# Kernel optimization log

Measured on AMD Instinct MI355X. Metric: run time of the kernel, lower is better.

The kernel has to match this reference:

```python
import jax, jax.numpy as jnp
import numpy as np

N, E, T, D, M, G = 131072, 524288, 4, 128, 256, 4096
VOCAB, GH, L, PASSES = 100, 512, 128, 4


def setup_inputs() -> dict:
    key = jax.random.key(0)
    ks = jax.random.split(key, 20)
    node_types = jax.random.randint(ks[0], (N,), 0, VOCAB)
    edge_src = jax.random.randint(ks[1], (E,), 0, N)
    edge_dst = jax.random.randint(ks[2], (E,), 0, N)
    edge_type = jax.random.randint(ks[3], (E,), 0, T)
    inner = jnp.sort(jax.random.randint(ks[4], (G - 1,), 0, N))
    ptr = jnp.concatenate([jnp.zeros((1,), jnp.int64 if inner.dtype == jnp.int64 else jnp.int32),
                           inner, jnp.full((1,), N, inner.dtype)])
    s = 1.0 / np.sqrt(D)
    emb = jax.random.normal(ks[5], (VOCAB, D), jnp.float32)
    W_msg = jax.random.normal(ks[6], (T, M, D), jnp.float32) * s
    b_msg = jax.random.normal(ks[7], (T, M), jnp.float32) * s
    W_ih = jax.random.normal(ks[8], (3 * D, M), jnp.float32) * (1.0 / np.sqrt(M))
    W_hh = jax.random.normal(ks[9], (3 * D, D), jnp.float32) * s
    b_ih = jax.random.normal(ks[10], (3 * D,), jnp.float32) * s
    b_hh = jax.random.normal(ks[11], (3 * D,), jnp.float32) * s
    W_gate = jax.random.normal(ks[12], (1, D), jnp.float32) * s
    b_gate = jax.random.normal(ks[13], (1,), jnp.float32) * s
    W_n2g = jax.random.normal(ks[14], (GH, D), jnp.float32) * s
    b_n2g = jax.random.normal(ks[15], (GH,), jnp.float32) * s
    W_loc = jax.random.normal(ks[16], (L, GH), jnp.float32) * (1.0 / np.sqrt(GH))
    b_loc = jax.random.normal(ks[17], (L,), jnp.float32) * (1.0 / np.sqrt(GH))
    W_lv = jax.random.normal(ks[18], (L, GH), jnp.float32) * (1.0 / np.sqrt(GH))
    b_lv = jax.random.normal(ks[19], (L,), jnp.float32) * (1.0 / np.sqrt(GH))
    return dict(node_types=node_types, edge_src=edge_src, edge_dst=edge_dst,
                edge_type=edge_type, ptr=ptr, emb=emb, W_msg=W_msg, b_msg=b_msg,
                W_ih=W_ih, W_hh=W_hh, b_ih=b_ih, b_hh=b_hh, W_gate=W_gate,
                b_gate=b_gate, W_n2g=W_n2g, b_n2g=b_n2g, W_loc=W_loc, b_loc=b_loc,
                W_lv=W_lv, b_lv=b_lv)


def _ggnn_pass(h, edge_src, edge_dst, edge_type, W_msg, b_msg, W_ih, W_hh, b_ih, b_hh):
    # per-edge-type linear on all nodes: [T, N, M]
    msgs_all = jnp.einsum('nd,tmd->tnm', h, W_msg) + b_msg[:, None, :]
    # gather the message of the edge's type at its source node: [E, M]
    e_msg = msgs_all[edge_type, edge_src]
    # sparse adjacency matmul == scatter-add of source messages into destinations
    agg = jax.ops.segment_sum(e_msg, edge_dst, num_segments=h.shape[0])
    m = jax.nn.relu(agg)
    # torch GRUCell
    gi = m @ W_ih.T + b_ih      # [N, 3D]
    gh = h @ W_hh.T + b_hh      # [N, 3D]
    d = h.shape[1]
    ir, iz, inn = gi[:, :d], gi[:, d:2 * d], gi[:, 2 * d:]
    hr, hz, hn = gh[:, :d], gh[:, d:2 * d], gh[:, 2 * d:]
    r = jax.nn.sigmoid(ir + hr)
    z = jax.nn.sigmoid(iz + hz)
    n = jnp.tanh(inn + r * hn)
    return (1.0 - z) * n + z * h


def reference(node_types, edge_src, edge_dst, edge_type, ptr, emb, W_msg, b_msg,
              W_ih, W_hh, b_ih, b_hh, W_gate, b_gate, W_n2g, b_n2g,
              W_loc, b_loc, W_lv, b_lv):
    h = emb[node_types]  # [N, D]
    for _ in range(PASSES):
        h = _ggnn_pass(h, edge_src, edge_dst, edge_type,
                       W_msg, b_msg, W_ih, W_hh, b_ih, b_hh)
    # gated segment readout (equivalent to per-graph attn @ h slices)
    gate = jax.nn.sigmoid(h @ W_gate.T + b_gate)        # [N, 1]
    hg = h @ W_n2g.T + b_n2g                            # [N, GH]
    seg = jnp.searchsorted(ptr, jnp.arange(h.shape[0]), side='right') - 1
    h_graph = jax.ops.segment_sum(gate * hg, seg, num_segments=ptr.shape[0] - 1)
    z_loc = h_graph @ W_loc.T + b_loc
    z_logvar = h_graph @ W_lv.T + b_lv
    return (z_loc, z_logvar)
```

## Files before the change

### kernel.cpp

```cpp
#include <hip/hip_runtime.h>
#include <cstdint>
#include <cstddef>

#define NN 131072
#define EE 524288
#define GG 4096
#define NPASS 4

typedef __attribute__((ext_vector_type(4))) float f32x4;
typedef __attribute__((ext_vector_type(8))) short bfrag;

__device__ __forceinline__ unsigned short f2bf(float f) {
  union { float f; unsigned u; } v; v.f = f;
  unsigned r = v.u + 0x7fffu + ((v.u >> 16) & 1u);
  return (unsigned short)(r >> 16);
}
__device__ __forceinline__ float bf2f(unsigned short h) {
  union { unsigned u; float f; } v; v.u = ((unsigned)h) << 16;
  return v.f;
}
__device__ __forceinline__ unsigned pack2(float x, float y) {
  return (unsigned)f2bf(x) | ((unsigned)f2bf(y) << 16);
}
__device__ __forceinline__ float sigm(float x) { return 1.f / (1.f + __expf(-x)); }
__device__ __forceinline__ float sigm_fast(float x) {
  return __builtin_amdgcn_rcpf(1.f + __expf(-x));
}
__device__ __forceinline__ float tanh_fast(float x) {
  return 1.f - 2.f * __builtin_amdgcn_rcpf(1.f + __expf(2.f * x));
}

__device__ __forceinline__ void cp16(unsigned short* l, const unsigned short* g) {
  __builtin_amdgcn_global_load_lds(
      (const __attribute__((address_space(1))) unsigned int*)g,
      (__attribute__((address_space(3))) unsigned int*)l, 16, 0, 0);
}

__global__ void prep_wb(const float* __restrict__ Wmsg, unsigned short* __restrict__ Wb) {
  int idx = blockIdx.x * 256 + threadIdx.x;
  if (idx >= 256 * 512) return;
  int m = idx >> 9, k = idx & 511;
  int t = k >> 7, d = k & 127;
  Wb[idx] = f2bf(Wmsg[((size_t)t * 256 + m) * 128 + d]);
}

__global__ void prep_wgru(const float* __restrict__ Wih, const float* __restrict__ Whh,
                          unsigned short* __restrict__ Wgru) {
  int idx = blockIdx.x * 256 + threadIdx.x;
  if (idx >= 512 * 384) return;
  int j = idx / 384, kk = idx % 384;
  float v;
  if (kk < 256) v = (j < 384) ? Wih[j * 256 + kk] : 0.f;
  else          v = (j < 256) ? Whh[j * 128 + (kk - 256)]
                   : ((j >= 384) ? Whh[(j - 128) * 128 + (kk - 256)] : 0.f);
  int g = (j < 128) ? 0 : (j < 256) ? 1 : (j < 384) ? 2 : 3;
  int d = j & 127;
  Wgru[(size_t)(4 * d + g) * 384 + kk] = f2bf(v);
}

__global__ void prep_bias(const float* __restrict__ bih, const float* __restrict__ bhh,
                          float* __restrict__ biasg) {
  int j = blockIdx.x * 256 + threadIdx.x;
  if (j >= 512) return;
  float v;
  if (j < 256) v = bih[j] + bhh[j];
  else if (j < 384) v = bih[j];
  else v = bhh[j - 128];
  int g = (j < 128) ? 0 : (j < 256) ? 1 : (j < 384) ? 2 : 3;
  int d = j & 127;
  biasg[4 * d + g] = v;
}

__global__ void compose_k(const float* __restrict__ Wloc, const float* __restrict__ Wlv,
                          const float* __restrict__ Wn2g, float* __restrict__ WcT) {
  int b = blockIdx.x;
  int jl = threadIdx.x >> 7, d = threadIdx.x & 127;
  int j = b * 2 + jl;
  const float* wx = (j < 128) ? Wloc + (size_t)j * 512 : Wlv + (size_t)(j - 128) * 512;
  float acc = 0.f;
  for (int k = 0; k < 512; k++) acc += wx[k] * Wn2g[k * 128 + d];
  WcT[d * 256 + j] = acc;
}

__global__ void cvec_k(const float* __restrict__ Wloc, const float* __restrict__ Wlv,
                       const float* __restrict__ bn2g, float* __restrict__ cvec) {
  int j = threadIdx.x;
  const float* wx = (j < 128) ? Wloc + (size_t)j * 512 : Wlv + (size_t)(j - 128) * 512;
  float a = 0.f;
  for (int k = 0; k < 512; k++) a += wx[k] * bn2g[k];
  cvec[j] = a;
}

__global__ void init_h(const int* __restrict__ nt, const float* __restrict__ emb,
                       unsigned short* __restrict__ H) {
  size_t idx = (size_t)blockIdx.x * 256 + threadIdx.x;
  int n = (int)(idx >> 7), d = (int)(idx & 127);
  H[idx] = f2bf(emb[(size_t)nt[n] * 128 + d]);
}

__global__ void cnt4_k(const int* __restrict__ edst, const int* __restrict__ etype,
                       int* __restrict__ cnti) {
  int e = blockIdx.x * 256 + threadIdx.x;
  if (e >= EE) return;
  atomicAdd(&cnti[edst[e] * 4 + etype[e]], 1);
}

__global__ void degsum_k(const int* __restrict__ cnti, int* __restrict__ deg,
                         float* __restrict__ cnt) {
  int n = blockIdx.x * 256 + threadIdx.x;
  if (n >= NN) return;
  int4 c4 = *(const int4*)&cnti[n * 4];
  deg[n] = c4.x + c4.y + c4.z + c4.w;
  float4 f4 = make_float4((float)c4.x, (float)c4.y, (float)c4.z, (float)c4.w);
  *(float4*)&cnt[n * 4] = f4;
}

__global__ __launch_bounds__(1024) void scan_k(const int* __restrict__ deg,
                                               int* __restrict__ rowptr,
                                               int* __restrict__ cursor) {
  __shared__ int part[1024];
  int t = threadIdx.x;
  int base = t * 128;
  const int4* deg4 = (const int4*)(deg + base);
  int s = 0;
#pragma unroll 8
  for (int i = 0; i < 32; i++) {
    int4 d = deg4[i];
    s += d.x + d.y + d.z + d.w;
  }
  part[t] = s;
  __syncthreads();
  for (int off = 1; off < 1024; off <<= 1) {
    int v = (t >= off) ? part[t - off] : 0;
    __syncthreads();
    part[t] += v;
    __syncthreads();
  }
  int run = part[t] - s;
#pragma unroll 8
  for (int i = 0; i < 32; i++) {
    int4 d = deg4[i];
    int4 rp;
    rp.x = run; run += d.x;
    rp.y = run; run += d.y;
    rp.z = run; run += d.z;
    rp.w = run; run += d.w;
    *(int4*)&rowptr[base + i * 4] = rp;
    *(int4*)&cursor[base + i * 4] = rp;
  }
  if (t == 1023) rowptr[NN] = run;
}

__global__ void fill_k(const int* __restrict__ esrc, const int* __restrict__ edst,
                       const int* __restrict__ etype, int* __restrict__ cursor,
                       unsigned* __restrict__ epack) {
  int e = blockIdx.x * 256 + threadIdx.x;
  if (e >= EE) return;
  int pos = atomicAdd(&cursor[edst[e]], 1);
  epack[pos] = ((unsigned)etype[e] << 17) | (unsigned)esrc[e];
}

__global__ __launch_bounds__(256) void agg_k(const int* __restrict__ rowptr,
                                             const unsigned* __restrict__ epack,
                                             const unsigned short* __restrict__ H,
                                             unsigned short* __restrict__ s) {
  int n = blockIdx.x * 4 + (threadIdx.x >> 6);
  int lane = threadIdx.x & 63;
  int half = lane >> 5;
  int l31 = lane & 31;
  int beg = rowptr[n], end = rowptr[n + 1];
  const unsigned short* hb = H + l31 * 4;
  float4 acc0 = {0.f, 0.f, 0.f, 0.f}, acc1 = {0.f, 0.f, 0.f, 0.f};
  float4 acc2 = {0.f, 0.f, 0.f, 0.f}, acc3 = {0.f, 0.f, 0.f, 0.f};

#define ACC2(P, HX, HY)                                                        \
  {                                                                            \
    int t_ = (int)((P) >> 17);                                                 \
    float u0 = bf2f((unsigned short)((HX) & 0xffffu));                         \
    float u1 = bf2f((unsigned short)((HX) >> 16));                             \
    float u2 = bf2f((unsigned short)((HY) & 0xffffu));                         \
    float u3 = bf2f((unsigned short)((HY) >> 16));                             \
    if (t_ == 0)      { acc0.x += u0; acc0.y += u1; acc0.z += u2; acc0.w += u3; } \
    else if (t_ == 1) { acc1.x += u0; acc1.y += u1; acc1.z += u2; acc1.w += u3; } \
    else if (t_ == 2) { acc2.x += u0; acc2.y += u1; acc2.z += u2; acc2.w += u3; } \
    else              { acc3.x += u0; acc3.y += u1; acc3.z += u2; acc3.w += u3; } \
  }

  for (int base = beg; base < end; base += 64) {
    int cnt = end - base;
    if (cnt > 64) cnt = 64;
    int mye = base + lane;
    unsigned ep = (mye < end) ? epack[mye] : 0u;
    for (int jb = 0; jb < cnt; jb += 4) {
      int rem = cnt - jb;
      int jA = jb + half;
      unsigned pA = (unsigned)__shfl((int)ep, jA);
      uint2 hA = make_uint2(0u, 0u);
      if (jA < cnt) hA = *(const uint2*)&hb[(size_t)(pA & 0x1FFFFu) * 128];
      unsigned pB = 0u;
      uint2 hB = make_uint2(0u, 0u);
      if (rem > 2) {
        int jB = jb + 2 + half;
        pB = (unsigned)__shfl((int)ep, jB);
        if (jB < cnt) hB = *(const uint2*)&hb[(size_t)(pB & 0x1FFFFu) * 128];
      }
      ACC2(pA, hA.x, hA.y);
      if (rem > 2) ACC2(pB, hB.x, hB.y);
    }
  }
#undef ACC2

  acc0.x += __shfl_xor(acc0.x, 32); acc0.y += __shfl_xor(acc0.y, 32);
  acc0.z += __shfl_xor(acc0.z, 32); acc0.w += __shfl_xor(acc0.w, 32);
  acc1.x += __shfl_xor(acc1.x, 32); acc1.y += __shfl_xor(acc1.y, 32);
  acc1.z += __shfl_xor(acc1.z, 32); acc1.w += __shfl_xor(acc1.w, 32);
  acc2.x += __shfl_xor(acc2.x, 32); acc2.y += __shfl_xor(acc2.y, 32);
  acc2.z += __shfl_xor(acc2.z, 32); acc2.w += __shfl_xor(acc2.w, 32);
  acc3.x += __shfl_xor(acc3.x, 32); acc3.y += __shfl_xor(acc3.y, 32);
  acc3.z += __shfl_xor(acc3.z, 32); acc3.w += __shfl_xor(acc3.w, 32);

  unsigned short* srow = s + (size_t)n * 512;
  {
    float4 va = half ? acc2 : acc0;
    int t0 = half ? 2 : 0;
    uint2 wv;
    wv.x = pack2(va.x, va.y); wv.y = pack2(va.z, va.w);
    *(uint2*)&srow[t0 * 128 + l31 * 4] = wv;
    float4 vb = half ? acc3 : acc1;
    int t1 = half ? 3 : 1;
    wv.x = pack2(vb.x, vb.y); wv.y = pack2(vb.z, vb.w);
    *(uint2*)&srow[t1 * 128 + l31 * 4] = wv;
  }
}

__global__ __launch_bounds__(512, 4) void msgemm_k(
    unsigned short* __restrict__ s, const float* __restrict__ cnt,
    const unsigned short* __restrict__ Wb, const float* __restrict__ bmsg) {
  __shared__ __align__(16) unsigned short As[2][128 * 32];
  __shared__ __align__(16) unsigned short Bs[2][256 * 32];
  int i0 = blockIdx.x * 128;
  int tid = threadIdx.x, lane = tid & 63, w = tid >> 6;
  int wi = w >> 1, wj = w & 1;
  int q = lane >> 4, r = lane & 15;
  int srow = tid >> 2;
  int swcol = ((tid & 3) ^ ((srow >> 1) & 3)) * 8;

  const unsigned short* sP = s + (size_t)(i0 + srow) * 512 + swcol;
  const unsigned short* WbP = Wb + (size_t)srow * 512 + swcol;

  int aoff[2], boff[8];
#pragma unroll
  for (int rt = 0; rt < 2; rt++) {
    int row = wi * 32 + rt * 16 + r;
    aoff[rt] = row * 32 + (q ^ ((row >> 1) & 3)) * 8;
  }
#pragma unroll
  for (int ct = 0; ct < 8; ct++) {
    int row = wj * 128 + ct * 16 + r;
    boff[ct] = row * 32 + (q ^ ((row >> 1) & 3)) * 8;
  }

  f32x4 acc[2][8];
#pragma unroll
  for (int a = 0; a < 2; a++)
#pragma unroll
    for (int b = 0; b < 8; b++) acc[a][b] = f32x4{0.f, 0.f, 0.f, 0.f};

  cp16(&As[0][w * 512], sP);
#pragma unroll
  for (int c = 0; c < 2; c++)
    cp16(&Bs[0][c * 4096 + w * 512], WbP + (size_t)(c * 128) * 512);

  for (int ks = 0; ks < 16; ks++) {
    int b = ks & 1;
    if (ks < 15) {
      int nb = b ^ 1;
      cp16(&As[nb][w * 512], sP + (ks + 1) * 32);
#pragma unroll
      for (int c = 0; c < 2; c++)
        cp16(&Bs[nb][c * 4096 + w * 512],
             WbP + (size_t)(c * 128) * 512 + (ks + 1) * 32);
      asm volatile("s_waitcnt vmcnt(3)" ::: "memory");
    } else {
      asm volatile("s_waitcnt vmcnt(0)" ::: "memory");
    }
    __builtin_amdgcn_s_barrier();
    __builtin_amdgcn_sched_barrier(0);
    bfrag af[2];
#pragma unroll
    for (int rt = 0; rt < 2; rt++) af[rt] = *(const bfrag*)&As[b][aoff[rt]];
#pragma unroll
    for (int ct = 0; ct < 8; ct++) {
      bfrag bfr = *(const bfrag*)&Bs[b][boff[ct]];
#pragma unroll
      for (int rt = 0; rt < 2; rt++)
        acc[rt][ct] =
            __builtin_amdgcn_mfma_f32_16x16x32_bf16(af[rt], bfr, acc[rt][ct], 0, 0, 0);
    }
    __builtin_amdgcn_sched_barrier(0);
    __builtin_amdgcn_s_barrier();
    __builtin_amdgcn_sched_barrier(0);
  }

#pragma unroll
  for (int ct = 0; ct < 8; ct++) {
    int j = wj * 128 + ct * 16 + r;
    float b0 = bmsg[j], b1 = bmsg[256 + j], b2 = bmsg[512 + j], b3 = bmsg[768 + j];
#pragma unroll
    for (int rt = 0; rt < 2; rt++) {
#pragma unroll
      for (int reg = 0; reg < 4; reg++) {
        int il = wi * 32 + rt * 16 + q * 4 + reg;
        float4 c4 = *(const float4*)&cnt[(size_t)(i0 + il) * 4];
        float v = acc[rt][ct][reg] + c4.x * b0 + c4.y * b1 + c4.z * b2 + c4.w * b3;
        v = v > 0.f ? v : 0.f;
        s[(size_t)(i0 + il) * 512 + j] = f2bf(v);
      }
    }
  }
}

__global__ __launch_bounds__(512, 4) void grugemm_k(
    const unsigned short* __restrict__ m,
    const unsigned short* __restrict__ Hc, unsigned short* __restrict__ Hn,
    const unsigned short* __restrict__ Wgru, const float* __restrict__ biasg) {
  __shared__ __align__(16) unsigned char smem[49152];
  unsigned short* As = (unsigned short*)smem;
  unsigned short* Bs = (unsigned short*)(smem + 16384);
  unsigned* pg = (unsigned*)smem;
  int wg = (blockIdx.x & 7) * 256 + (blockIdx.x >> 3);
  int bcol = wg & 1;
  int i0 = (wg >> 1) * 128;
  int tid = threadIdx.x, lane = tid & 63, w = tid >> 6;
  int wi = w >> 1, wj = w & 1;
  int q = lane >> 4, r = lane & 15;
  int srow = tid >> 2;
  int swcol = ((tid & 3) ^ ((srow >> 1) & 3)) * 8;

  const unsigned short* mP = m + (size_t)(i0 + srow) * 512 + swcol;
  const unsigned short* hP = Hc + (size_t)(i0 + srow) * 128 + swcol;
  const unsigned short* WgP = Wgru + (size_t)(bcol * 256 + srow) * 384 + swcol;

  int aoff[2], boff[8];
#pragma unroll
  for (int rt = 0; rt < 2; rt++) {
    int row = wi * 32 + rt * 16 + r;
    aoff[rt] = row * 32 + (q ^ ((row >> 1) & 3)) * 8;
  }
#pragma unroll
  for (int ct = 0; ct < 8; ct++) {
    int row = wj * 128 + ct * 16 + r;
    boff[ct] = row * 32 + (q ^ ((row >> 1) & 3)) * 8;
  }

  f32x4 acc[2][8];
#pragma unroll
  for (int a = 0; a < 2; a++)
#pragma unroll
    for (int b = 0; b < 8; b++) acc[a][b] = f32x4{0.f, 0.f, 0.f, 0.f};

  cp16(&As[0 * 4096 + w * 512], mP);
#pragma unroll
  for (int c = 0; c < 2; c++)
    cp16(&Bs[0 * 8192 + c * 4096 + w * 512], WgP + (size_t)(c * 128) * 384);

  for (int ks = 0; ks < 12; ks++) {
    int b = ks & 1;
    if (ks < 11) {
      int nb = b ^ 1;
      int nks = ks + 1;
      const unsigned short* aSrc =
          (nks < 8) ? (mP + nks * 32) : (hP + (nks - 8) * 32);
      cp16(&As[nb * 4096 + w * 512], aSrc);
#pragma unroll
      for (int c = 0; c < 2; c++)
        cp16(&Bs[nb * 8192 + c * 4096 + w * 512],
             WgP + (size_t)(c * 128) * 384 + nks * 32);
      asm volatile("s_waitcnt vmcnt(3)" ::: "memory");
    } else {
      asm volatile("s_waitcnt vmcnt(0)" ::: "memory");
    }
    __builtin_amdgcn_s_barrier();
    __builtin_amdgcn_sched_barrier(0);
    bfrag af[2];
#pragma unroll
    for (int rt = 0; rt < 2; rt++) af[rt] = *(const bfrag*)&As[b * 4096 + aoff[rt]];
#pragma unroll
    for (int ct = 0; ct < 8; ct++) {
      bfrag bfr = *(const bfrag*)&Bs[b * 8192 + boff[ct]];
#pragma unroll
      for (int rt = 0; rt < 2; rt++)
        acc[rt][ct] =
            __builtin_amdgcn_mfma_f32_16x16x32_bf16(af[rt], bfr, acc[rt][ct], 0, 0, 0);
    }
    __builtin_amdgcn_sched_barrier(0);
    __builtin_amdgcn_s_barrier();
    __builtin_amdgcn_sched_barrier(0);
  }

  int rr = r & 3;
  bool s1 = (lane & 1) != 0, s2 = (lane & 2) != 0;
#pragma unroll
  for (int ct = 0; ct < 8; ct++) {
    float bias = biasg[bcol * 256 + wj * 128 + ct * 16 + r];
    int dl = wj * 32 + ct * 4 + (r >> 2);
#pragma unroll
    for (int rt = 0; rt < 2; rt++) {
      float v0 = acc[rt][ct][0] + bias;
      float v1 = acc[rt][ct][1] + bias;
      float v2 = acc[rt][ct][2] + bias;
      float v3 = acc[rt][ct][3] + bias;
      float t, rcv;
      t = s1 ? v0 : v1; rcv = __shfl_xor(t, 1);
      v0 = s1 ? rcv : v0; v1 = s1 ? v1 : rcv;
      t = s1 ? v2 : v3; rcv = __shfl_xor(t, 1);
      v2 = s1 ? rcv : v2; v3 = s1 ? v3 : rcv;
      t = s2 ? v0 : v2; rcv = __shfl_xor(t, 2);
      v0 = s2 ? rcv : v0; v2 = s2 ? v2 : rcv;
      t = s2 ? v1 : v3; rcv = __shfl_xor(t, 2);
      v1 = s2 ? rcv : v1; v3 = s2 ? v3 : rcv;
      int il = wi * 32 + rt * 16 + q * 4 + rr;
      float rg = sigm_fast(v0), zg = sigm_fast(v1);
      float ng = tanh_fast(v2 + rg * v3);
      pg[il * 66 + dl] = pack2((1.f - zg) * ng, zg);
    }
  }
  __syncthreads();

#pragma unroll
  for (int half = 0; half < 2; half++) {
    int row = half * 64 + (tid >> 3);
    int c0 = (tid & 7) * 8;
    size_t gbase = (size_t)(i0 + row) * 128 + bcol * 64 + c0;
    bfrag hv8 = *(const bfrag*)&Hc[gbase];
    uint4 p0 = *(const uint4*)&pg[row * 66 + c0];
    uint4 p1 = *(const uint4*)&pg[row * 66 + c0 + 4];
    unsigned pw[8] = {p0.x, p0.y, p0.z, p0.w, p1.x, p1.y, p1.z, p1.w};
    bfrag outv;
#pragma unroll
    for (int e = 0; e < 8; e++) {
      float a = bf2f((unsigned short)(pw[e] & 0xffffu));
      float z = bf2f((unsigned short)(pw[e] >> 16));
      float hold = bf2f((unsigned short)hv8[e]);
      outv[e] = (short)f2bf(a + z * hold);
    }
    *(bfrag*)&Hn[gbase] = outv;
  }
}

__global__ __launch_bounds__(256) void gate_k(const unsigned short* __restrict__ H,
                                              const float* __restrict__ Wg,
                                              const float* __restrict__ bg,
                                              float* __restrict__ gate) {
  __shared__ float wg[128];
  if (threadIdx.x < 128) wg[threadIdx.x] = Wg[threadIdx.x];
  __syncthreads();
  int g = threadIdx.x >> 4, sub = threadIdx.x & 15;
  int n = blockIdx.x * 16 + g;
  const unsigned short* hr = H + (size_t)n * 128;
  float p = 0.f;
  for (int k = sub; k < 128; k += 16) p += bf2f(hr[k]) * wg[k];
  p += __shfl_xor(p, 1);
  p += __shfl_xor(p, 2);
  p += __shfl_xor(p, 4);
  p += __shfl_xor(p, 8);
  if (sub == 0) gate[n] = sigm(p + bg[0]);
}

__global__ __launch_bounds__(256) void gsum_k(const unsigned short* __restrict__ H,
                                              const float* __restrict__ gate,
                                              const int* __restrict__ ptr,
                                              float* __restrict__ gsum,
                                              float* __restrict__ sg) {
  int g = blockIdx.x * 4 + (threadIdx.x >> 6);
  int lane = threadIdx.x & 63;
  int start = ptr[g], end = ptr[g + 1];
  float a0 = 0.f, a1 = 0.f, gs = 0.f;
  int n = start;
  for (; n + 4 <= end; n += 4) {
    float g0 = gate[n], g1 = gate[n + 1], g2 = gate[n + 2], g3 = gate[n + 3];
    unsigned v0 = *(const unsigned*)&H[(size_t)n * 128 + lane * 2];
    unsigned v1 = *(const unsigned*)&H[(size_t)(n + 1) * 128 + lane * 2];
    unsigned v2 = *(const unsigned*)&H[(size_t)(n + 2) * 128 + lane * 2];
    unsigned v3 = *(const unsigned*)&H[(size_t)(n + 3) * 128 + lane * 2];
    a0 += g0 * bf2f((unsigned short)(v0 & 0xffffu)) +
          g1 * bf2f((unsigned short)(v1 & 0xffffu)) +
          g2 * bf2f((unsigned short)(v2 & 0xffffu)) +
          g3 * bf2f((unsigned short)(v3 & 0xffffu));
    a1 += g0 * bf2f((unsigned short)(v0 >> 16)) +
          g1 * bf2f((unsigned short)(v1 >> 16)) +
          g2 * bf2f((unsigned short)(v2 >> 16)) +
          g3 * bf2f((unsigned short)(v3 >> 16));
    gs += g0 + g1 + g2 + g3;
  }
  for (; n < end; n++) {
    float gt = gate[n];
    unsigned hv = *(const unsigned*)&H[(size_t)n * 128 + lane * 2];
    a0 += gt * bf2f((unsigned short)(hv & 0xffffu));
    a1 += gt * bf2f((unsigned short)(hv >> 16));
    gs += gt;
  }
  gsum[(size_t)g * 128 + lane * 2] = a0;
  gsum[(size_t)g * 128 + lane * 2 + 1] = a1;
  if (lane == 0) sg[g] = gs;
}

__global__ __launch_bounds__(256) void zfinal_k(const float* __restrict__ gsum,
                                                const float* __restrict__ sg,
                                                const float* __restrict__ WcT,
                                                const float* __restrict__ cvec,
                                                const float* __restrict__ bloc,
                                                const float* __restrict__ blv,
                                                float* __restrict__ out) {
  __shared__ float gs[128];
  __shared__ float sgs;
  int g = blockIdx.x;
  int j = threadIdx.x;
  if (j < 128) gs[j] = gsum[(size_t)g * 128 + j];
  if (j == 0) sgs = sg[g];
  __syncthreads();
  float acc = (j < 128 ? bloc[j] : blv[j - 128]) + sgs * cvec[j];
  for (int d = 0; d < 128; d++) acc += gs[d] * WcT[d * 256 + j];
  size_t o = (j < 128) ? ((size_t)g * 128 + j)
                       : ((size_t)GG * 128 + (size_t)g * 128 + (j - 128));
  out[o] = acc;
}

extern "C" void kernel_launch(void* const* d_in, const int* in_sizes, int n_in,
                              void* d_out, int out_size, void* d_ws, size_t ws_size,
                              hipStream_t stream) {
  const int* node_types = (const int*)d_in[0];
  const int* esrc = (const int*)d_in[1];
  const int* edst = (const int*)d_in[2];
  const int* etype = (const int*)d_in[3];
  const int* ptr = (const int*)d_in[4];
  const float* emb = (const float*)d_in[5];
  const float* Wmsg = (const float*)d_in[6];
  const float* bmsg = (const float*)d_in[7];
  const float* Wih = (const float*)d_in[8];
  const float* Whh = (const float*)d_in[9];
  const float* bih = (const float*)d_in[10];
  const float* bhh = (const float*)d_in[11];
  const float* Wg = (const float*)d_in[12];
  const float* bg = (const float*)d_in[13];
  const float* Wn2g = (const float*)d_in[14];
  const float* bn2g = (const float*)d_in[15];
  const float* Wloc = (const float*)d_in[16];
  const float* bloc = (const float*)d_in[17];
  const float* Wlv = (const float*)d_in[18];
  const float* blv = (const float*)d_in[19];
  float* out = (float*)d_out;

  char* ws = (char*)d_ws;
  size_t off = 0;
  unsigned short* s = (unsigned short*)(ws);
  off += (size_t)NN * 512 * 2;
  unsigned short* H0 = (unsigned short*)(ws + off);
  off += (size_t)NN * 128 * 2;
  unsigned short* H1 = (unsigned short*)(ws + off);
  off += (size_t)NN * 128 * 2;
  float* cnt = (float*)(ws + off);
  off += (size_t)NN * 4 * 4;
  int* cnti = (int*)(ws + off);
  off += (size_t)NN * 4 * 4;
  int* deg = (int*)(ws + off);
  off += (size_t)NN * 4;
  int* rowptr = (int*)(ws + off);
  off += (size_t)(NN + 64) * 4;
  int* cursor = (int*)(ws + off);
  off += (size_t)NN * 4;
  unsigned* epack = (unsigned*)(ws + off);
  off += (size_t)EE * 4;
  float* gate = (float*)(ws + off);
  off += (size_t)NN * 4;
  float* gsum = (float*)(ws + off);
  off += (size_t)GG * 128 * 4;
  float* sg = (float*)(ws + off);
  off += (size_t)GG * 4;
  float* WcT = (float*)(ws + off);
  off += 128 * 256 * 4;
  float* cvec = (float*)(ws + off);
  off += 256 * 4;
  unsigned short* Wb = (unsigned short*)(ws + off);
  off += 256 * 512 * 2;
  unsigned short* Wgru = (unsigned short*)(ws + off);
  off += 512 * 384 * 2;
  float* biasg = (float*)(ws + off);
  off += 512 * 4;

  hipMemsetAsync(cnti, 0, (size_t)NN * 16, stream);
  prep_wb<<<512, 256, 0, stream>>>(Wmsg, Wb);
  prep_wgru<<<768, 256, 0, stream>>>(Wih, Whh, Wgru);
  prep_bias<<<2, 256, 0, stream>>>(bih, bhh, biasg);
  compose_k<<<128, 256, 0, stream>>>(Wloc, Wlv, Wn2g, WcT);
  cvec_k<<<1, 256, 0, stream>>>(Wloc, Wlv, bn2g, cvec);
  init_h<<<NN * 128 / 256, 256, 0, stream>>>(node_types, emb, H0);
  cnt4_k<<<EE / 256, 256, 0, stream>>>(edst, etype, cnti);
  degsum_k<<<NN / 256, 256, 0, stream>>>(cnti, deg, cnt);
  scan_k<<<1, 1024, 0, stream>>>(deg, rowptr, cursor);
  fill_k<<<EE / 256, 256, 0, stream>>>(esrc, edst, etype, cursor, epack);

  unsigned short* Hc = H0;
  unsigned short* Hn = H1;
  for (int p = 0; p < NPASS; p++) {
    agg_k<<<NN / 4, 256, 0, stream>>>(rowptr, epack, Hc, s);
    msgemm_k<<<NN / 128, 512, 0, stream>>>(s, cnt, Wb, bmsg);
    grugemm_k<<<NN / 128 * 2, 512, 0, stream>>>(s, Hc, Hn, Wgru, biasg);
    unsigned short* tmp = Hc; Hc = Hn; Hn = tmp;
  }

  gate_k<<<NN / 16, 256, 0, stream>>>(Hc, Wg, bg, gate);
  gsum_k<<<GG / 4, 256, 0, stream>>>(Hc, gate, ptr, gsum, sg);
  zfinal_k<<<GG, 256, 0, stream>>>(gsum, sg, WcT, cvec, bloc, blv, out);
}
```

Baseline: 1.082 ms.

## Fuse edge aggregation into message GEMM kernel per 128-node tile

Merges the per-node gather/aggregation kernel into the message GEMM kernel. Each of the 8 waves aggregates 16 nodes serially, writes them to global s, then the block syncs and runs the GEMM on the same tile. This saves one launch per pass and should keep the s tile warm in cache. In exchange, aggregation parallelism drops (one wave handles 16 nodes serially, 1024 blocks instead of 32768), so latency hiding for the random gathers may suffer.

```diff
diff --git a/kernel.cpp b/kernel.cpp
--- a/kernel.cpp
+++ b/kernel.cpp
@@ -160,19 +160,20 @@
   epack[pos] = ((unsigned)etype[e] << 17) | (unsigned)esrc[e];
 }
 
-__global__ __launch_bounds__(256) void agg_k(const int* __restrict__ rowptr,
-                                             const unsigned* __restrict__ epack,
-                                             const unsigned short* __restrict__ H,
-                                             unsigned short* __restrict__ s) {
-  int n = blockIdx.x * 4 + (threadIdx.x >> 6);
-  int lane = threadIdx.x & 63;
-  int half = lane >> 5;
-  int l31 = lane & 31;
-  int beg = rowptr[n], end = rowptr[n + 1];
-  const unsigned short* hb = H + l31 * 4;
-  float4 acc0 = {0.f, 0.f, 0.f, 0.f}, acc1 = {0.f, 0.f, 0.f, 0.f};
-  float4 acc2 = {0.f, 0.f, 0.f, 0.f}, acc3 = {0.f, 0.f, 0.f, 0.f};
-
+__global__ __launch_bounds__(512, 4) void aggmm_k(
+    const int* __restrict__ rowptr, const unsigned* __restrict__ epack,
+    const unsigned short* __restrict__ Hc,
+    unsigned short* __restrict__ s, const float* __restrict__ cnt,
+    const unsigned short* __restrict__ Wb, const float* __restrict__ bmsg) {
+  __shared__ __align__(16) unsigned short As[2][128 * 32];
+  __shared__ __align__(16) unsigned short Bs[2][256 * 32];
+  int i0 = blockIdx.x * 128;
+  int tid = threadIdx.x, lane = tid & 63, w = tid >> 6;
+
+  {
+    int half = lane >> 5;
+    int l31 = lane & 31;
+    const unsigned short* hb = Hc + l31 * 4;
 #define ACC2(P, HX, HY)                                                        \
   {                                                                            \
     int t_ = (int)((P) >> 17);                                                 \
@@ -185,61 +186,57 @@
     else if (t_ == 2) { acc2.x += u0; acc2.y += u1; acc2.z += u2; acc2.w += u3; } \
     else              { acc3.x += u0; acc3.y += u1; acc3.z += u2; acc3.w += u3; } \
   }
-
-  for (int base = beg; base < end; base += 64) {
-    int cnt = end - base;
-    if (cnt > 64) cnt = 64;
-    int mye = base + lane;
-    unsigned ep = (mye < end) ? epack[mye] : 0u;
-    for (int jb = 0; jb < cnt; jb += 4) {
-      int rem = cnt - jb;
-      int jA = jb + half;
-      unsigned pA = (unsigned)__shfl((int)ep, jA);
-      uint2 hA = make_uint2(0u, 0u);
-      if (jA < cnt) hA = *(const uint2*)&hb[(size_t)(pA & 0x1FFFFu) * 128];
-      unsigned pB = 0u;
-      uint2 hB = make_uint2(0u, 0u);
-      if (rem > 2) {
-        int jB = jb + 2 + half;
-        pB = (unsigned)__shfl((int)ep, jB);
-        if (jB < cnt) hB = *(const uint2*)&hb[(size_t)(pB & 0x1FFFFu) * 128];
+    for (int ni = 0; ni < 16; ni++) {
+      int n = i0 + w * 16 + ni;
+      int beg = rowptr[n], end = rowptr[n + 1];
+      float4 acc0 = {0.f, 0.f, 0.f, 0.f}, acc1 = {0.f, 0.f, 0.f, 0.f};
+      float4 acc2 = {0.f, 0.f, 0.f, 0.f}, acc3 = {0.f, 0.f, 0.f, 0.f};
+      for (int base = beg; base < end; base += 64) {
+        int cnt_ = end - base;
+        if (cnt_ > 64) cnt_ = 64;
+        int mye = base + lane;
+        unsigned ep = (mye < end) ? epack[mye] : 0u;
+        for (int jb = 0; jb < cnt_; jb += 4) {
+          int rem = cnt_ - jb;
+          int jA = jb + half;
+          unsigned pA = (unsigned)__shfl((int)ep, jA);
+          uint2 hA = make_uint2(0u, 0u);
+          if (jA < cnt_) hA = *(const uint2*)&hb[(size_t)(pA & 0x1FFFFu) * 128];
+          unsigned pB = 0u;
+          uint2 hB = make_uint2(0u, 0u);
+          if (rem > 2) {
+            int jB = jb + 2 + half;
+            pB = (unsigned)__shfl((int)ep, jB);
+            if (jB < cnt_) hB = *(const uint2*)&hb[(size_t)(pB & 0x1FFFFu) * 128];
+          }
+          ACC2(pA, hA.x, hA.y);
+          if (rem > 2) ACC2(pB, hB.x, hB.y);
+        }
       }
-      ACC2(pA, hA.x, hA.y);
-      if (rem > 2) ACC2(pB, hB.x, hB.y);
-    }
-  }
+      acc0.x += __shfl_xor(acc0.x, 32); acc0.y += __shfl_xor(acc0.y, 32);
+      acc0.z += __shfl_xor(acc0.z, 32); acc0.w += __shfl_xor(acc0.w, 32);
+      acc1.x += __shfl_xor(acc1.x, 32); acc1.y += __shfl_xor(acc1.y, 32);
+      acc1.z += __shfl_xor(acc1.z, 32); acc1.w += __shfl_xor(acc1.w, 32);
+      acc2.x += __shfl_xor(acc2.x, 32); acc2.y += __shfl_xor(acc2.y, 32);
+      acc2.z += __shfl_xor(acc2.z, 32); acc2.w += __shfl_xor(acc2.w, 32);
+      acc3.x += __shfl_xor(acc3.x, 32); acc3.y += __shfl_xor(acc3.y, 32);
+      acc3.z += __shfl_xor(acc3.z, 32); acc3.w += __shfl_xor(acc3.w, 32);
+      unsigned short* srow = s + (size_t)n * 512;
+      float4 va = half ? acc2 : acc0;
+      int t0 = half ? 2 : 0;
+      uint2 wv;
+      wv.x = pack2(va.x, va.y); wv.y = pack2(va.z, va.w);
+      *(uint2*)&srow[t0 * 128 + l31 * 4] = wv;
+      float4 vb = half ? acc3 : acc1;
+      int t1 = half ? 3 : 1;
+      wv.x = pack2(vb.x, vb.y); wv.y = pack2(vb.z, vb.w);
+      *(uint2*)&srow[t1 * 128 + l31 * 4] = wv;
+    }
 #undef ACC2
-
-  acc0.x += __shfl_xor(acc0.x, 32); acc0.y += __shfl_xor(acc0.y, 32);
-  acc0.z += __shfl_xor(acc0.z, 32); acc0.w += __shfl_xor(acc0.w, 32);
-  acc1.x += __shfl_xor(acc1.x, 32); acc1.y += __shfl_xor(acc1.y, 32);
-  acc1.z += __shfl_xor(acc1.z, 32); acc1.w += __shfl_xor(acc1.w, 32);
-  acc2.x += __shfl_xor(acc2.x, 32); acc2.y += __shfl_xor(acc2.y, 32);
-  acc2.z += __shfl_xor(acc2.z, 32); acc2.w += __shfl_xor(acc2.w, 32);
-  acc3.x += __shfl_xor(acc3.x, 32); acc3.y += __shfl_xor(acc3.y, 32);
-  acc3.z += __shfl_xor(acc3.z, 32); acc3.w += __shfl_xor(acc3.w, 32);
-
-  unsigned short* srow = s + (size_t)n * 512;
-  {
-    float4 va = half ? acc2 : acc0;
-    int t0 = half ? 2 : 0;
-    uint2 wv;
-    wv.x = pack2(va.x, va.y); wv.y = pack2(va.z, va.w);
-    *(uint2*)&srow[t0 * 128 + l31 * 4] = wv;
-    float4 vb = half ? acc3 : acc1;
-    int t1 = half ? 3 : 1;
-    wv.x = pack2(vb.x, vb.y); wv.y = pack2(vb.z, vb.w);
-    *(uint2*)&srow[t1 * 128 + l31 * 4] = wv;
-  }
-}
-
-__global__ __launch_bounds__(512, 4) void msgemm_k(
-    unsigned short* __restrict__ s, const float* __restrict__ cnt,
-    const unsigned short* __restrict__ Wb, const float* __restrict__ bmsg) {
-  __shared__ __align__(16) unsigned short As[2][128 * 32];
-  __shared__ __align__(16) unsigned short Bs[2][256 * 32];
-  int i0 = blockIdx.x * 128;
-  int tid = threadIdx.x, lane = tid & 63, w = tid >> 6;
+  }
+  asm volatile("s_waitcnt vmcnt(0)" ::: "memory");
+  __syncthreads();
+
   int wi = w >> 1, wj = w & 1;
   int q = lane >> 4, r = lane & 15;
   int srow = tid >> 2;
@@ -603,8 +600,7 @@
   unsigned short* Hc = H0;
   unsigned short* Hn = H1;
   for (int p = 0; p < NPASS; p++) {
-    agg_k<<<NN / 4, 256, 0, stream>>>(rowptr, epack, Hc, s);
-    msgemm_k<<<NN / 128, 512, 0, stream>>>(s, cnt, Wb, bmsg);
+    aggmm_k<<<NN / 128, 512, 0, stream>>>(rowptr, epack, Hc, s, cnt, Wb, bmsg);
     grugemm_k<<<NN / 128 * 2, 512, 0, stream>>>(s, Hc, Hn, Wgru, biasg);
     unsigned short* tmp = Hc; Hc = Hn; Hn = tmp;
   }
```

Measured after the change: 1.132 ms. +4.6%, slower.
